# Optimization experiments

Measured on AMD Instinct MI355X. Metric: run time of the kernel, lower is better.

The kernel has to match this reference:

```python
import jax, jax.numpy as jnp
import numpy as np

B, S, D, H = 2, 2048, 1024, 16
DK = D // H


def setup_inputs() -> dict:
    key = jax.random.key(0)
    ks = jax.random.split(key, 7)
    return {
        "query": jax.random.normal(ks[0], (B, S, D), jnp.float32),
        "key": jax.random.normal(ks[1], (B, S, D), jnp.float32),
        "value": jax.random.normal(ks[2], (B, S, D), jnp.float32),
        "w_q": jax.random.normal(ks[3], (D, D), jnp.float32) * (1.0 / np.sqrt(D)),
        "w_k": jax.random.normal(ks[4], (D, D), jnp.float32) * (1.0 / np.sqrt(D)),
        "w_v": jax.random.normal(ks[5], (D, D), jnp.float32) * (1.0 / np.sqrt(D)),
        "w_o": jax.random.normal(ks[6], (D, D), jnp.float32) * (1.0 / np.sqrt(D)),
    }


def reference(query, key, value, w_q, w_k, w_v, w_o):
    # Linear(bias=False) in torch computes x @ W.T where W is [out, in].
    Q = jnp.einsum('bsd,ed->bse', query, w_q)
    K = jnp.einsum('bsd,ed->bse', key, w_k)
    V = jnp.einsum('bsd,ed->bse', value, w_v)
    # split heads: [B, H, S, DK]
    Q = Q.reshape(B, S, H, DK).transpose(0, 2, 1, 3)
    K = K.reshape(B, S, H, DK).transpose(0, 2, 1, 3)
    V = V.reshape(B, S, H, DK).transpose(0, 2, 1, 3)
    scale = 1.0 / np.sqrt(DK).astype(np.float32)
    scores = jnp.einsum('bhqd,bhkd->bhqk', Q, K) * scale  # [B,H,S,S]
    attn = jax.nn.softmax(scores, axis=-1)
    context = jnp.einsum('bhqk,bhkd->bhqd', attn, V)
    context = context.transpose(0, 2, 1, 3).reshape(B, S, D)
    return jnp.einsum('bsd,ed->bse', context, w_o)
```

## Files before the change

kernel.cpp:

```cpp
#include <hip/hip_runtime.h>

typedef unsigned short u16;
typedef unsigned int u32;
typedef __bf16 bf16x8 __attribute__((ext_vector_type(8)));
typedef float f32x4 __attribute__((ext_vector_type(4)));
typedef short s16x4 __attribute__((ext_vector_type(4)));

#define AS1 __attribute__((address_space(1)))
#define AS3 __attribute__((address_space(3)))

__device__ __forceinline__ f32x4 mfma16(bf16x8 a, bf16x8 b, f32x4 c) {
    return __builtin_amdgcn_mfma_f32_16x16x32_bf16(a, b, c, 0, 0, 0);
}
__device__ __forceinline__ f32x4 mfma16k16(s16x4 a, s16x4 b, f32x4 c) {
    return __builtin_amdgcn_mfma_f32_16x16x16bf16_1k(a, b, c, 0, 0, 0);
}

__device__ __forceinline__ u16 f2bf(float f) {
    return __builtin_bit_cast(u16, (__bf16)f);
}

__device__ __forceinline__ void gld16(const u16* g, u16* l) {
    __builtin_amdgcn_global_load_lds((AS1 void*)g, (AS3 void*)l, 16, 0, 0);
}

__global__ __launch_bounds__(256) void cvt_all(const float* __restrict__ q, const float* __restrict__ k,
                                               const float* __restrict__ v, const float* __restrict__ wq,
                                               const float* __restrict__ wk, const float* __restrict__ wv,
                                               const float* __restrict__ wo, u16* __restrict__ qo,
                                               u16* __restrict__ ko, u16* __restrict__ vo,
                                               u16* __restrict__ wqo, u16* __restrict__ wko,
                                               u16* __restrict__ wvo, u16* __restrict__ woo) {
    const int y = blockIdx.y;
    const float* x; u16* o; int n;
    switch (y) {
        case 0: x = q; o = qo; n = 4 << 20; break;
        case 1: x = k; o = ko; n = 4 << 20; break;
        case 2: x = v; o = vo; n = 4 << 20; break;
        case 3: x = wq; o = wqo; n = 1 << 20; break;
        case 4: x = wk; o = wko; n = 1 << 20; break;
        case 5: x = wv; o = wvo; n = 1 << 20; break;
        default: x = wo; o = woo; n = 1 << 20; break;
    }
    int i = (blockIdx.x * 256 + threadIdx.x) * 4;
    if (i >= n) return;
    float4 vv = *(const float4*)(x + i);
    u32 lo = (u32)f2bf(vv.x) | ((u32)f2bf(vv.y) << 16);
    u32 hi = (u32)f2bf(vv.z) | ((u32)f2bf(vv.w) << 16);
    *(uint2*)(o + i) = make_uint2(lo, hi);
}

template <int BM, int BN, bool BF16OUT>
__device__ __forceinline__ void gemm_core(const u16* __restrict__ A, const u16* __restrict__ Bt,
                                          void* __restrict__ Cp, int K, int N, int m0, int n0,
                                          float oscale) {
    constexpr int WROWS = BM / 64;
    constexpr int WCOLS = 4 / WROWS;
    constexpr int BFR = BN / WCOLS / 16;
    __shared__ __align__(16) u16 As[BM * 32];
    __shared__ __align__(16) u16 Bs[BN * 32];
    const int tid = threadIdx.x;
    const int lane = tid & 63, wave = tid >> 6;
    const int l16 = lane & 15, q4 = lane >> 4;
    const int wm = (wave / WCOLS) * 64, wn = (wave % WCOLS) * (BFR * 16);

    const f32x4 fz = {0.f, 0.f, 0.f, 0.f};
    f32x4 acc[4][BFR];
#pragma unroll
    for (int i = 0; i < 4; ++i)
#pragma unroll
        for (int j = 0; j < BFR; ++j) acc[i][j] = fz;

    const int rseg = lane >> 2;
    const int ck = ((lane & 3) ^ ((lane >> 3) & 3)) * 8;
    const u16* Ag = A + (size_t)(m0 + wave * 16 + rseg) * K + ck;
    const u16* Bg = Bt + (size_t)(n0 + wave * 16 + rseg) * K + ck;

    const int swz = (q4 ^ ((l16 & 7) >> 1)) * 8;

    for (int k0 = 0; k0 < K; k0 += 32) {
        __syncthreads();
#pragma unroll
        for (int p = 0; p < BM / 64; ++p)
            gld16(Ag + (size_t)p * 64 * K + k0, As + p * 2048 + wave * 512);
#pragma unroll
        for (int p = 0; p < BN / 64; ++p)
            gld16(Bg + (size_t)p * 64 * K + k0, Bs + p * 2048 + wave * 512);
        __syncthreads();
        bf16x8 af[4], bfr[BFR];
#pragma unroll
        for (int i = 0; i < 4; ++i)
            af[i] = *(const bf16x8*)&As[(wm + i * 16 + l16) * 32 + swz];
#pragma unroll
        for (int j = 0; j < BFR; ++j)
            bfr[j] = *(const bf16x8*)&Bs[(wn + j * 16 + l16) * 32 + swz];
#pragma unroll
        for (int i = 0; i < 4; ++i)
#pragma unroll
            for (int j = 0; j < BFR; ++j) acc[i][j] = mfma16(af[i], bfr[j], acc[i][j]);
    }

#pragma unroll
    for (int i = 0; i < 4; ++i) {
        const int row = m0 + wm + i * 16 + q4 * 4;
#pragma unroll
        for (int j = 0; j < BFR; ++j) {
            const int col = n0 + wn + j * 16 + l16;
#pragma unroll
            for (int r = 0; r < 4; ++r) {
                const float vr = acc[i][j][r] * oscale;
                if constexpr (BF16OUT)
                    ((u16*)Cp)[(size_t)(row + r) * N + col] = f2bf(vr);
                else
                    ((float*)Cp)[(size_t)(row + r) * N + col] = vr;
            }
        }
    }
}

__global__ __launch_bounds__(256) void gemm_qkv(const u16* __restrict__ qb, const u16* __restrict__ kb,
                                                const u16* __restrict__ vb, const u16* __restrict__ wqb,
                                                const u16* __restrict__ wkb, const u16* __restrict__ wvb,
                                                u16* __restrict__ Qp, u16* __restrict__ Kp,
                                                u16* __restrict__ VtAll) {
    const int z = blockIdx.y, x = blockIdx.x;
    const u16 *A, *Bt;
    u16* C;
    int N, m0, n0;
    float sc = 1.0f;
    if (z == 0) {
        A = qb; Bt = wqb; C = Qp; N = 1024; m0 = (x >> 3) * 128; n0 = (x & 7) * 128;
        sc = 0.18033688011112042f;
    } else if (z == 1) {
        A = kb; Bt = wkb; C = Kp; N = 1024; m0 = (x >> 3) * 128; n0 = (x & 7) * 128;
    } else {
        A = wvb; Bt = vb; C = VtAll; N = 4096; m0 = (x >> 5) * 128; n0 = (x & 31) * 128;
    }
    gemm_core<128, 128, true>(A, Bt, C, 1024, N, m0, n0, sc);
}

__global__ __launch_bounds__(256) void gemm_out(const u16* __restrict__ ctx,
                                                const u16* __restrict__ wob,
                                                float* __restrict__ out) {
    const int x = blockIdx.x;
    gemm_core<64, 128, false>(ctx, wob, out, 1024, 1024, (x >> 3) * 64, (x & 7) * 128, 1.0f);
}

__global__ __launch_bounds__(256) void flash_attn(const u16* __restrict__ Qp,
                                                  const u16* __restrict__ Kp,
                                                  const u16* __restrict__ VtAll,
                                                  u16* __restrict__ Ctx) {
    constexpr int D = 1024, SS = 2048, LD = 72;
    __shared__ __align__(16) u16 Ks[2][64 * LD];
    __shared__ __align__(16) u16 Vts[2][64 * LD];

    const int tid = threadIdx.x;
    const int lane = tid & 63, wave = tid >> 6;
    const int l16 = lane & 15, q4 = lane >> 4;
    const int h = blockIdx.y, b = blockIdx.z;
    const int q0 = blockIdx.x * 128 + wave * 32;

    bf16x8 qf[2][2];
#pragma unroll
    for (int qs = 0; qs < 2; ++qs) {
        const u16* Qb = Qp + (size_t)(b * SS + q0 + qs * 16 + l16) * D + h * 64;
        qf[qs][0] = *(const bf16x8*)(Qb + q4 * 8);
        qf[qs][1] = *(const bf16x8*)(Qb + 32 + q4 * 8);
    }

    const f32x4 fz = {0.f, 0.f, 0.f, 0.f};
    f32x4 ot[2][4], lacc[2];
    lacc[0] = fz; lacc[1] = fz;
#pragma unroll
    for (int qs = 0; qs < 2; ++qs)
#pragma unroll
        for (int dt = 0; dt < 4; ++dt) ot[qs][dt] = fz;

    s16x4 onesA;
    onesA[0] = onesA[1] = onesA[2] = onesA[3] = (short)0x3F80;

    const int sr = tid >> 3, scol = (tid & 7) * 8;
    const int vswap = wave & 1;
    const int swV = (l16 >> 3) & 1;
    const u16* Kg = Kp + (size_t)(b * SS + sr) * D + h * 64 + scol;
    const u16* Vg = VtAll + (size_t)(h * 64 + sr) * 4096 + b * SS + scol;

    uint4 k0v = *(const uint4*)(Kg);
    uint4 k1v = *(const uint4*)(Kg + (size_t)32 * D);
    uint4 v0v = *(const uint4*)(Vg);
    uint4 v1v = *(const uint4*)(Vg + (size_t)32 * 4096);

    for (int kt = 0; kt < SS; kt += 64) {
        const int buf = (kt >> 6) & 1;
        uint4 w0 = v0v, w1 = v1v;
        if (vswap) {
            w0 = make_uint4(v0v.z, v0v.w, v0v.x, v0v.y);
            w1 = make_uint4(v1v.z, v1v.w, v1v.x, v1v.y);
        }
        *(uint4*)&Ks[buf][sr * LD + scol] = k0v;
        *(uint4*)&Ks[buf][(sr + 32) * LD + scol] = k1v;
        *(uint4*)&Vts[buf][sr * LD + scol] = w0;
        *(uint4*)&Vts[buf][(sr + 32) * LD + scol] = w1;

        const int nk = (kt + 64 < SS) ? kt + 64 : 0;
        k0v = *(const uint4*)(Kg + (size_t)nk * D);
        k1v = *(const uint4*)(Kg + (size_t)(nk + 32) * D);
        v0v = *(const uint4*)(Vg + nk);
        v1v = *(const uint4*)(Vg + (size_t)32 * 4096 + nk);

        __syncthreads();

        f32x4 st[2][4];
#pragma unroll
        for (int nt = 0; nt < 4; ++nt) {
            const bf16x8 ka = *(const bf16x8*)&Ks[buf][(nt * 16 + l16) * LD + q4 * 8];
            const bf16x8 kbf = *(const bf16x8*)&Ks[buf][(nt * 16 + l16) * LD + 32 + q4 * 8];
#pragma unroll
            for (int qs = 0; qs < 2; ++qs) {
                f32x4 s = mfma16(ka, qf[qs][0], fz);
                st[qs][nt] = mfma16(kbf, qf[qs][1], s);
            }
        }
        s16x4 p[2][4];
#pragma unroll
        for (int qs = 0; qs < 2; ++qs)
#pragma unroll
            for (int nt = 0; nt < 4; ++nt) {
                s16x4 pk;
#pragma unroll
                for (int r = 0; r < 4; ++r)
                    pk[r] = (short)f2bf(__builtin_amdgcn_exp2f(st[qs][nt][r]));
                p[qs][nt] = pk;
            }
#pragma unroll
        for (int nt = 0; nt < 4; ++nt) {
#pragma unroll
            for (int dt = 0; dt < 4; ++dt) {
                const s16x4 va =
                    *(const s16x4*)&Vts[buf][(dt * 16 + l16) * LD + ((nt * 4 + q4) ^ swV) * 4];
                ot[0][dt] = mfma16k16(va, p[0][nt], ot[0][dt]);
                ot[1][dt] = mfma16k16(va, p[1][nt], ot[1][dt]);
            }
            lacc[0] = mfma16k16(onesA, p[0][nt], lacc[0]);
            lacc[1] = mfma16k16(onesA, p[1][nt], lacc[1]);
        }
    }

#pragma unroll
    for (int qs = 0; qs < 2; ++qs) {
        const float inv = 1.f / lacc[qs][0];
        u16* Cb = Ctx + (size_t)(b * SS + q0 + qs * 16 + l16) * D + h * 64 + q4 * 4;
#pragma unroll
        for (int dt = 0; dt < 4; ++dt) {
            s16x4 w;
#pragma unroll
            for (int r = 0; r < 4; ++r) w[r] = (short)f2bf(ot[qs][dt][r] * inv);
            *(s16x4*)(Cb + dt * 16) = w;
        }
    }
}

extern "C" void kernel_launch(void* const* d_in, const int* in_sizes, int n_in,
                              void* d_out, int out_size, void* d_ws, size_t ws_size,
                              hipStream_t stream) {
    const float* query = (const float*)d_in[0];
    const float* key   = (const float*)d_in[1];
    const float* value = (const float*)d_in[2];
    const float* w_q   = (const float*)d_in[3];
    const float* w_k   = (const float*)d_in[4];
    const float* w_v   = (const float*)d_in[5];
    const float* w_o   = (const float*)d_in[6];
    float* out = (float*)d_out;

    const size_t MEG = 1024 * 1024;
    if (ws_size < 64 * MEG) return;
    u16* ws = (u16*)d_ws;
    u16* qb    = ws;
    u16* kb    = ws + 4 * MEG;
    u16* vb    = ws + 8 * MEG;
    u16* wqb   = ws + 12 * MEG;
    u16* wkb   = ws + 13 * MEG;
    u16* wvb   = ws + 14 * MEG;
    u16* wob   = ws + 15 * MEG;
    u16* Qp    = ws + 16 * MEG;
    u16* Kp    = ws + 20 * MEG;
    u16* VtAll = ws + 24 * MEG;
    u16* ctx   = ws + 28 * MEG;

    cvt_all<<<dim3(4096, 7), 256, 0, stream>>>(query, key, value, w_q, w_k, w_v, w_o,
                                               qb, kb, vb, wqb, wkb, wvb, wob);
    gemm_qkv<<<dim3(256, 3), 256, 0, stream>>>(qb, kb, vb, wqb, wkb, wvb, Qp, Kp, VtAll);
    flash_attn<<<dim3(16, 16, 2), 256, 0, stream>>>(Qp, Kp, VtAll, ctx);
    gemm_out<<<dim3(512), 256, 0, stream>>>(ctx, wob, out);
}
```

Before: 218.1 us.

## Split flash attention across eight waves, swizzle block order, relax barrier

```diff
diff --git a/kernel.cpp b/kernel.cpp
--- a/kernel.cpp
+++ b/kernel.cpp
@@ -22,6 +22,12 @@
 
 __device__ __forceinline__ void gld16(const u16* g, u16* l) {
     __builtin_amdgcn_global_load_lds((AS1 void*)g, (AS3 void*)l, 16, 0, 0);
+}
+
+__device__ __forceinline__ void barrier_nodrain() {
+    asm volatile("s_waitcnt lgkmcnt(0)" ::: "memory");
+    __builtin_amdgcn_s_barrier();
+    asm volatile("" ::: "memory");
 }
 
 __global__ __launch_bounds__(256) void cvt_all(const float* __restrict__ q, const float* __restrict__ k,
@@ -123,7 +129,9 @@
                                                 const u16* __restrict__ wkb, const u16* __restrict__ wvb,
                                                 u16* __restrict__ Qp, u16* __restrict__ Kp,
                                                 u16* __restrict__ VtAll) {
-    const int z = blockIdx.y, x = blockIdx.x;
+    const int z = blockIdx.y;
+    int x = blockIdx.x;
+    if (z != 2) x = (x & 7) * 32 + (x >> 3);
     const u16 *A, *Bt;
     u16* C;
     int N, m0, n0;
@@ -142,14 +150,14 @@
 __global__ __launch_bounds__(256) void gemm_out(const u16* __restrict__ ctx,
                                                 const u16* __restrict__ wob,
                                                 float* __restrict__ out) {
-    const int x = blockIdx.x;
-    gemm_core<64, 128, false>(ctx, wob, out, 1024, 1024, (x >> 3) * 64, (x & 7) * 128, 1.0f);
-}
-
-__global__ __launch_bounds__(256) void flash_attn(const u16* __restrict__ Qp,
-                                                  const u16* __restrict__ Kp,
-                                                  const u16* __restrict__ VtAll,
-                                                  u16* __restrict__ Ctx) {
+    const int xo = (blockIdx.x & 7) * 64 + (blockIdx.x >> 3);
+    gemm_core<64, 128, false>(ctx, wob, out, 1024, 1024, (xo >> 3) * 64, (xo & 7) * 128, 1.0f);
+}
+
+__global__ __launch_bounds__(512, 4) void flash_attn(const u16* __restrict__ Qp,
+                                                     const u16* __restrict__ Kp,
+                                                     const u16* __restrict__ VtAll,
+                                                     u16* __restrict__ Ctx) {
     constexpr int D = 1024, SS = 2048, LD = 72;
     __shared__ __align__(16) u16 Ks[2][64 * LD];
     __shared__ __align__(16) u16 Vts[2][64 * LD];
@@ -157,104 +165,94 @@
     const int tid = threadIdx.x;
     const int lane = tid & 63, wave = tid >> 6;
     const int l16 = lane & 15, q4 = lane >> 4;
-    const int h = blockIdx.y, b = blockIdx.z;
-    const int q0 = blockIdx.x * 128 + wave * 32;
-
-    bf16x8 qf[2][2];
-#pragma unroll
-    for (int qs = 0; qs < 2; ++qs) {
-        const u16* Qb = Qp + (size_t)(b * SS + q0 + qs * 16 + l16) * D + h * 64;
-        qf[qs][0] = *(const bf16x8*)(Qb + q4 * 8);
-        qf[qs][1] = *(const bf16x8*)(Qb + 32 + q4 * 8);
+
+    const int nb = blockIdx.x;
+    const int orig = (nb & 7) * 64 + (nb >> 3);
+    const int h = (orig >> 4) & 15, b = orig >> 8;
+    const int q0 = (orig & 15) * 128 + wave * 16;
+
+    bf16x8 qf[2];
+    {
+        const u16* Qb = Qp + (size_t)(b * SS + q0 + l16) * D + h * 64;
+        qf[0] = *(const bf16x8*)(Qb + q4 * 8);
+        qf[1] = *(const bf16x8*)(Qb + 32 + q4 * 8);
     }
 
     const f32x4 fz = {0.f, 0.f, 0.f, 0.f};
-    f32x4 ot[2][4], lacc[2];
-    lacc[0] = fz; lacc[1] = fz;
-#pragma unroll
-    for (int qs = 0; qs < 2; ++qs)
-#pragma unroll
-        for (int dt = 0; dt < 4; ++dt) ot[qs][dt] = fz;
+    f32x4 ot[4], lacc = fz;
+#pragma unroll
+    for (int dt = 0; dt < 4; ++dt) ot[dt] = fz;
 
     s16x4 onesA;
     onesA[0] = onesA[1] = onesA[2] = onesA[3] = (short)0x3F80;
 
-    const int sr = tid >> 3, scol = (tid & 7) * 8;
-    const int vswap = wave & 1;
+    const int sr = tid >> 3;
+    const int scol = (tid & 7) * 8;
+    const int vswap = (sr >> 3) & 1;
     const int swV = (l16 >> 3) & 1;
     const u16* Kg = Kp + (size_t)(b * SS + sr) * D + h * 64 + scol;
     const u16* Vg = VtAll + (size_t)(h * 64 + sr) * 4096 + b * SS + scol;
 
-    uint4 k0v = *(const uint4*)(Kg);
-    uint4 k1v = *(const uint4*)(Kg + (size_t)32 * D);
-    uint4 v0v = *(const uint4*)(Vg);
-    uint4 v1v = *(const uint4*)(Vg + (size_t)32 * 4096);
-
+    uint4 kv, vv;
+    auto prefetch = [&](int kt) {
+        kv = *(const uint4*)(Kg + (size_t)kt * D);
+        vv = *(const uint4*)(Vg + kt);
+    };
+    auto stage = [&](int buf) {
+        uint4 w = vswap ? make_uint4(vv.z, vv.w, vv.x, vv.y) : vv;
+        *(uint4*)&Ks[buf][sr * LD + scol] = kv;
+        *(uint4*)&Vts[buf][sr * LD + scol] = w;
+    };
+
+    prefetch(0);
     for (int kt = 0; kt < SS; kt += 64) {
         const int buf = (kt >> 6) & 1;
-        uint4 w0 = v0v, w1 = v1v;
-        if (vswap) {
-            w0 = make_uint4(v0v.z, v0v.w, v0v.x, v0v.y);
-            w1 = make_uint4(v1v.z, v1v.w, v1v.x, v1v.y);
-        }
-        *(uint4*)&Ks[buf][sr * LD + scol] = k0v;
-        *(uint4*)&Ks[buf][(sr + 32) * LD + scol] = k1v;
-        *(uint4*)&Vts[buf][sr * LD + scol] = w0;
-        *(uint4*)&Vts[buf][(sr + 32) * LD + scol] = w1;
-
+        stage(buf);
         const int nk = (kt + 64 < SS) ? kt + 64 : 0;
-        k0v = *(const uint4*)(Kg + (size_t)nk * D);
-        k1v = *(const uint4*)(Kg + (size_t)(nk + 32) * D);
-        v0v = *(const uint4*)(Vg + nk);
-        v1v = *(const uint4*)(Vg + (size_t)32 * 4096 + nk);
-
-        __syncthreads();
-
-        f32x4 st[2][4];
+        prefetch(nk);
+        barrier_nodrain();
+
+        f32x4 st[4];
+        __builtin_amdgcn_s_setprio(1);
 #pragma unroll
         for (int nt = 0; nt < 4; ++nt) {
             const bf16x8 ka = *(const bf16x8*)&Ks[buf][(nt * 16 + l16) * LD + q4 * 8];
-            const bf16x8 kbf = *(const bf16x8*)&Ks[buf][(nt * 16 + l16) * LD + 32 + q4 * 8];
-#pragma unroll
-            for (int qs = 0; qs < 2; ++qs) {
-                f32x4 s = mfma16(ka, qf[qs][0], fz);
-                st[qs][nt] = mfma16(kbf, qf[qs][1], s);
-            }
-        }
-        s16x4 p[2][4];
-#pragma unroll
-        for (int qs = 0; qs < 2; ++qs)
-#pragma unroll
-            for (int nt = 0; nt < 4; ++nt) {
-                s16x4 pk;
-#pragma unroll
-                for (int r = 0; r < 4; ++r)
-                    pk[r] = (short)f2bf(__builtin_amdgcn_exp2f(st[qs][nt][r]));
-                p[qs][nt] = pk;
-            }
+            const bf16x8 kb2 = *(const bf16x8*)&Ks[buf][(nt * 16 + l16) * LD + 32 + q4 * 8];
+            f32x4 s = mfma16(ka, qf[0], fz);
+            st[nt] = mfma16(kb2, qf[1], s);
+        }
+        __builtin_amdgcn_s_setprio(0);
+
+        s16x4 p[4];
+#pragma unroll
+        for (int nt = 0; nt < 4; ++nt) {
+#pragma unroll
+            for (int r = 0; r < 4; ++r)
+                p[nt][r] = (short)f2bf(__builtin_amdgcn_exp2f(st[nt][r]));
+        }
+
+        __builtin_amdgcn_s_setprio(1);
 #pragma unroll
         for (int nt = 0; nt < 4; ++nt) {
 #pragma unroll
             for (int dt = 0; dt < 4; ++dt) {
                 const s16x4 va =
                     *(const s16x4*)&Vts[buf][(dt * 16 + l16) * LD + ((nt * 4 + q4) ^ swV) * 4];
-                ot[0][dt] = mfma16k16(va, p[0][nt], ot[0][dt]);
-                ot[1][dt] = mfma16k16(va, p[1][nt], ot[1][dt]);
+                ot[dt] = mfma16k16(va, p[nt], ot[dt]);
             }
-            lacc[0] = mfma16k16(onesA, p[0][nt], lacc[0]);
-            lacc[1] = mfma16k16(onesA, p[1][nt], lacc[1]);
-        }
-    }
-
-#pragma unroll
-    for (int qs = 0; qs < 2; ++qs) {
-        const float inv = 1.f / lacc[qs][0];
-        u16* Cb = Ctx + (size_t)(b * SS + q0 + qs * 16 + l16) * D + h * 64 + q4 * 4;
+            lacc = mfma16k16(onesA, p[nt], lacc);
+        }
+        __builtin_amdgcn_s_setprio(0);
+    }
+
+    {
+        const float inv = 1.f / lacc[0];
+        u16* Cb = Ctx + (size_t)(b * SS + q0 + l16) * D + h * 64 + q4 * 4;
 #pragma unroll
         for (int dt = 0; dt < 4; ++dt) {
             s16x4 w;
 #pragma unroll
-            for (int r = 0; r < 4; ++r) w[r] = (short)f2bf(ot[qs][dt][r] * inv);
+            for (int r = 0; r < 4; ++r) w[r] = (short)f2bf(ot[dt][r] * inv);
             *(s16x4*)(Cb + dt * 16) = w;
         }
     }
@@ -290,6 +288,6 @@
     cvt_all<<<dim3(4096, 7), 256, 0, stream>>>(query, key, value, w_q, w_k, w_v, w_o,
                                                qb, kb, vb, wqb, wkb, wvb, wob);
     gemm_qkv<<<dim3(256, 3), 256, 0, stream>>>(qb, kb, vb, wqb, wkb, wvb, Qp, Kp, VtAll);
-    flash_attn<<<dim3(16, 16, 2), 256, 0, stream>>>(Qp, Kp, VtAll, ctx);
+    flash_attn<<<dim3(512), 512, 0, stream>>>(Qp, Kp, VtAll, ctx);
     gemm_out<<<dim3(512), 256, 0, stream>>>(ctx, wob, out);
 }
```

New measurement: 214.2 us. Within noise of the previous version (-1.8%).
